# Kernel tuning notes

Hardware: AMD Instinct MI355X
Metric: run time of the kernel (lower is better)

The kernel has to match this reference:

```python
import jax, jax.numpy as jnp
import numpy as np

N_NODES = 50000
N_EDGES = 800000
F_IN = 32
HID = 64
K = 4  # Chebyshev order in GConvLSTM(node_features, hidden, 4)


def setup_inputs() -> dict:
    key = jax.random.key(0)
    ks = jax.random.split(key, 14)
    x = jax.random.normal(ks[0], (N_NODES, F_IN), dtype=jnp.float32)
    edge_index = jax.random.randint(ks[1], (2, N_EDGES), 0, N_NODES, dtype=jnp.int64)
    edge_weight = jax.random.uniform(ks[2], (N_EDGES,), dtype=jnp.float32)
    s = 0.05
    # gate order: i, f, c, o
    Wx = jax.random.normal(ks[3], (4, K, F_IN, HID), dtype=jnp.float32) * s  # ChebConv weights on x
    bx = jax.random.normal(ks[4], (4, HID), dtype=jnp.float32) * s          # ChebConv biases on x
    Wh = jax.random.normal(ks[5], (4, K, HID, HID), dtype=jnp.float32) * s  # ChebConv weights on h
    bh = jax.random.normal(ks[6], (4, HID), dtype=jnp.float32) * s          # ChebConv biases on h
    wc = jax.random.normal(ks[7], (3, HID), dtype=jnp.float32) * s          # peephole w_c_i, w_c_f, w_c_o
    bg = jax.random.normal(ks[8], (4, HID), dtype=jnp.float32) * s          # gate biases b_i, b_f, b_c, b_o
    lin_w = jax.random.normal(ks[9], (HID, 1), dtype=jnp.float32) * s
    lin_b = jax.random.normal(ks[10], (1,), dtype=jnp.float32) * s
    return {"x": x, "edge_index": edge_index, "edge_weight": edge_weight,
            "Wx": Wx, "bx": bx, "Wh": Wh, "bh": bh, "wc": wc, "bg": bg,
            "lin_w": lin_w, "lin_b": lin_b}


def _cheb_norm(edge_index, edge_weight, num_nodes):
    # ChebConv.__norm__, sym normalization, lambda_max=2.0:
    # L_hat off-diagonal = -D^{-1/2} A D^{-1/2}, diagonal = 0.
    src, dst = edge_index[0], edge_index[1]
    deg = jax.ops.segment_sum(edge_weight, src, num_segments=num_nodes)
    d_inv_sqrt = jnp.where(deg > 0, jax.lax.rsqrt(jnp.maximum(deg, 1e-30)), 0.0)
    norm = -d_inv_sqrt[src] * edge_weight * d_inv_sqrt[dst]
    return src, dst, norm


def _cheb_conv(v, src, dst, norm, W, b, num_nodes):
    # ChebConv forward: out = sum_k T_k(L_hat) v @ W[k] + b, with propagate
    # = segment_sum of norm * v[src] at dst.
    def prop(t):
        return jax.ops.segment_sum(norm[:, None] * t[src], dst, num_segments=num_nodes)
    Tx0 = v
    out = Tx0 @ W[0]
    Tx1 = prop(Tx0)
    out = out + Tx1 @ W[1]
    for k in range(2, W.shape[0]):
        Tx2 = 2.0 * prop(Tx1) - Tx0
        out = out + Tx2 @ W[k]
        Tx0, Tx1 = Tx1, Tx2
    return out + b


def reference(x, edge_index, edge_weight, Wx, bx, Wh, bh, wc, bg, lin_w, lin_b):
    N = x.shape[0]
    src, dst, norm = _cheb_norm(edge_index, edge_weight, N)
    H = jnp.zeros((N, Wh.shape[-1]), dtype=x.dtype)
    C = jnp.zeros((N, Wh.shape[-1]), dtype=x.dtype)

    def gate(g, v_state):
        return (_cheb_conv(x, src, dst, norm, Wx[g], bx[g], N)
                + _cheb_conv(v_state, src, dst, norm, Wh[g], bh[g], N))

    I = jax.nn.sigmoid(gate(0, H) + wc[0] * C + bg[0])
    F = jax.nn.sigmoid(gate(1, H) + wc[1] * C + bg[1])
    T = jnp.tanh(gate(2, H) + bg[2])
    C = F * C + I * T
    O = jax.nn.sigmoid(gate(3, H) + wc[2] * C + bg[3])
    H = O * jnp.tanh(C)
    # dropout(p=0.25) is identity at inference; linear head HID -> 1
    return H @ lin_w + lin_b
```

## Files before the change

### kernel.cpp

```cpp
#include <hip/hip_runtime.h>
#include <math.h>


#define NT 256
#define NCH 64
#define RSH 20480
#define RSF 20480

typedef __attribute__((ext_vector_type(8))) short short8v;
typedef __attribute__((ext_vector_type(8))) unsigned short ushort8v;
typedef __attribute__((ext_vector_type(4))) float f32x4;

__device__ __forceinline__ short f2bf(float f) {
    unsigned u = __float_as_uint(f);
    u += 0x7FFFu + ((u >> 16) & 1u);
    return (short)(u >> 16);
}
__device__ __forceinline__ float bf2f(unsigned short b) {
    return __uint_as_float((unsigned)b << 16);
}

__global__ __launch_bounds__(1024)
void k_front(const int* __restrict__ src, const int* __restrict__ dst,
             const float* __restrict__ w, float* __restrict__ degPart,
             unsigned short* __restrict__ cntPart,
             const float* __restrict__ Wx, short* __restrict__ P,
             const float* __restrict__ x, short* __restrict__ xb,
             int nE, int N, int histB, int n4) {
    __shared__ float    s_deg[RSH];
    __shared__ unsigned s_cnt2[RSH / 2];
    const int bid = blockIdx.x;
    if (bid >= histB) {
        int idx = (bid - histB) * 1024 + (int)threadIdx.x;
        if (idx < 12 * 4 * 64) {
            int lane = idx & 63;
            int kt = (idx >> 6) & 3;
            int nt = idx >> 8;
            int gate = (nt < 4) ? 0 : (nt < 8) ? 2 : 3;
            int h = (nt & 3) * 16 + (lane & 15);
            int fb = (lane >> 4) * 8;
            short8v v;
#pragma unroll
            for (int j = 0; j < 8; ++j)
                v[j] = f2bf(Wx[((size_t)(gate * 4 + kt) * 32 + fb + j) * 64 + h]);
            *(reinterpret_cast<short8v*>(P) + idx) = v;
            return;
        }
        int i = idx - 12 * 4 * 64;
        if (i >= n4) return;
        const float4 v = *reinterpret_cast<const float4*>(x + (size_t)i * 4);
        short4 rb;
        rb.x = f2bf(v.x); rb.y = f2bf(v.y); rb.z = f2bf(v.z); rb.w = f2bf(v.w);
        *reinterpret_cast<short4*>(xb + (size_t)i * 4) = rb;
        return;
    }
    const int r = bid / NCH, b = bid % NCH;
    const int base = r * RSH;
    for (int i = threadIdx.x; i < RSH; i += 1024) s_deg[i] = 0.f;
    for (int i = threadIdx.x; i < RSH / 2; i += 1024) s_cnt2[i] = 0u;
    __syncthreads();
    const int chunk = (nE + NCH - 1) / NCH;
    const int e0 = b * chunk, e1 = min(e0 + chunk, nE);
    for (int e = e0 + (int)threadIdx.x; e < e1; e += 1024) {
        int s = src[e], d = dst[e];
        unsigned so = (unsigned)(s - base), dof = (unsigned)(d - base);
        if (so < RSH) atomicAdd(&s_deg[so], w[e]);
        if (dof < RSH) atomicAdd(&s_cnt2[dof >> 1], 1u << ((dof & 1) * 16));
    }
    __syncthreads();
    const int lim = min(RSH, N - base);
    for (int i = threadIdx.x; i < lim; i += 1024)
        degPart[(size_t)b * N + base + i] = s_deg[i];
    unsigned* cp32 = reinterpret_cast<unsigned*>(cntPart + (size_t)b * N + base);
    const int pairs = lim >> 1;
    for (int i = threadIdx.x; i < pairs; i += 1024) cp32[i] = s_cnt2[i];
    if ((lim & 1) && threadIdx.x == 0)
        cntPart[(size_t)b * N + base + lim - 1] =
            (unsigned short)(s_cnt2[lim >> 1] & 0xFFFFu);
}

__global__ __launch_bounds__(NT)
void k_scan_merged(const float* __restrict__ degPart,
                   const unsigned short* __restrict__ cntPart,
                   float* __restrict__ dinv, int* __restrict__ cnt,
                   int* __restrict__ rowptr, int* __restrict__ partials,
                   int* __restrict__ flag, int* __restrict__ offs, int N) {
    __shared__ unsigned s_c[NCH * NT];
    __shared__ int sp[NT];
    const int t = threadIdx.x;
    const int n0 = blockIdx.x * (NT * 2) + t * 2;
    float d0 = 0.f, d1 = 0.f;
    int c0 = 0, c1 = 0;
    if (n0 < N) {
#pragma unroll 8
        for (int b = 0; b < NCH; ++b) {
            const float2 dv = *reinterpret_cast<const float2*>(degPart + (size_t)b * N + n0);
            d0 += dv.x; d1 += dv.y;
            unsigned cc = *reinterpret_cast<const unsigned*>(cntPart + (size_t)b * N + n0);
            s_c[b * NT + t] = cc;
            c0 += (int)(cc & 0xFFFFu); c1 += (int)(cc >> 16);
        }
        dinv[n0] = d0 > 0.f ? rsqrtf(d0) : 0.f;
        cnt[n0] = c0;
        if (n0 + 1 < N) {
            dinv[n0 + 1] = d1 > 0.f ? rsqrtf(d1) : 0.f;
            cnt[n0 + 1] = c1;
        } else c1 = 0;
    }
    int cs = c0 + c1;
    sp[t] = cs;
    __syncthreads();
    for (int off = 1; off < NT; off <<= 1) {
        int u = (t >= off) ? sp[t - off] : 0;
        __syncthreads();
        sp[t] += u;
        __syncthreads();
    }
    const int ex = sp[t] - cs;
    const int total = sp[NT - 1];
    __syncthreads();
    if (t == 0) {
        __hip_atomic_store(&partials[blockIdx.x], total, __ATOMIC_RELEASE,
                           __HIP_MEMORY_SCOPE_AGENT);
        atomicAdd(flag, 1);
        while (__hip_atomic_load(flag, __ATOMIC_ACQUIRE,
                                 __HIP_MEMORY_SCOPE_AGENT) < (int)gridDim.x)
            __builtin_amdgcn_s_sleep(1);
    }
    __syncthreads();
    int v = (t < (int)blockIdx.x)
                ? __hip_atomic_load(&partials[t], __ATOMIC_ACQUIRE,
                                    __HIP_MEMORY_SCOPE_AGENT)
                : 0;
    sp[t] = v;
    __syncthreads();
    for (int off = NT / 2; off > 0; off >>= 1) {
        if (t < off) sp[t] += sp[t + off];
        __syncthreads();
    }
    const int prefix = sp[0];
    if (n0 >= N) return;
    const bool has1 = (n0 + 1) < N;
    int s0 = ex + prefix;
    int s1 = has1 ? ex + c0 + prefix : 0;
    rowptr[n0] = s0;
    if (has1) rowptr[n0 + 1] = s1;
#pragma unroll 8
    for (int b = 0; b < NCH; ++b) {
        unsigned cc = s_c[b * NT + t];
        if (has1) {
            *reinterpret_cast<int2*>(offs + (size_t)b * N + n0) = make_int2(s0, s1);
        } else {
            offs[(size_t)b * N + n0] = s0;
        }
        s0 += (int)(cc & 0xFFFFu);
        s1 += (int)(cc >> 16);
    }
}

__global__ __launch_bounds__(1024)
void k_fill2(const int* __restrict__ src, const int* __restrict__ dst,
             const float* __restrict__ w, const float* __restrict__ dinv,
             const int* __restrict__ offs, int2* __restrict__ entries,
             int nE, int N) {
    __shared__ int s_cur[RSF];
    const int r = blockIdx.x / NCH, b = blockIdx.x % NCH;
    const int base = r * RSF;
    const int lim = min(RSF, N - base);
    for (int i = threadIdx.x; i < lim; i += 1024)
        s_cur[i] = offs[(size_t)b * N + base + i];
    __syncthreads();
    const int chunk = (nE + NCH - 1) / NCH;
    const int e0 = b * chunk, e1 = min(e0 + chunk, nE);
    for (int e = e0 + (int)threadIdx.x; e < e1; e += 1024) {
        int d = dst[e];
        unsigned dof = (unsigned)(d - base);
        if (dof < RSF) {
            int s = src[e];
            float nv = -dinv[s] * w[e] * dinv[d];
            int pos = atomicAdd(&s_cur[dof], 1);
            entries[pos] = make_int2(s, __float_as_int(nv));
        }
    }
}

__device__ __forceinline__ void bf8_fma(float* acc, ushort8v v, float s) {
#pragma unroll
    for (int j = 0; j < 8; ++j)
        acc[j] = fmaf(s, bf2f(v[j]), acc[j]);
}

__global__ __launch_bounds__(256)
void k_gather_bf(const unsigned short* __restrict__ tb,
                 const unsigned short* __restrict__ subb,
                 short* __restrict__ outb,
                 const int* __restrict__ rowptr, const int* __restrict__ cnt,
                 const int2* __restrict__ entries, float scale, int N) {
    int idx = blockIdx.x * blockDim.x + threadIdx.x;
    if (idx >= N * 16) return;
    int n = idx >> 4, tq = idx & 3, qr = (idx >> 2) & 3;
    int beg = rowptr[n], end = beg + cnt[n];
    float acc0[8] = {0, 0, 0, 0, 0, 0, 0, 0};
    float acc1[8] = {0, 0, 0, 0, 0, 0, 0, 0};
    int i = beg + qr;
    for (; i + 12 < end; i += 16) {
        int2 e0 = entries[i];
        int2 e1 = entries[i + 4];
        int2 e2 = entries[i + 8];
        int2 e3 = entries[i + 12];
        ushort8v v0 = *reinterpret_cast<const ushort8v*>(tb + (size_t)e0.x * 32 + tq * 8);
        ushort8v v1 = *reinterpret_cast<const ushort8v*>(tb + (size_t)e1.x * 32 + tq * 8);
        ushort8v v2 = *reinterpret_cast<const ushort8v*>(tb + (size_t)e2.x * 32 + tq * 8);
        ushort8v v3 = *reinterpret_cast<const ushort8v*>(tb + (size_t)e3.x * 32 + tq * 8);
        bf8_fma(acc0, v0, __int_as_float(e0.y));
        bf8_fma(acc1, v1, __int_as_float(e1.y));
        bf8_fma(acc0, v2, __int_as_float(e2.y));
        bf8_fma(acc1, v3, __int_as_float(e3.y));
    }
    for (; i < end; i += 4) {
        int2 e0 = entries[i];
        ushort8v v0 = *reinterpret_cast<const ushort8v*>(tb + (size_t)e0.x * 32 + tq * 8);
        bf8_fma(acc0, v0, __int_as_float(e0.y));
    }
    float r[8];
#pragma unroll
    for (int j = 0; j < 8; ++j) {
        r[j] = acc0[j] + acc1[j];
        r[j] += __shfl_xor(r[j], 4);
        r[j] += __shfl_xor(r[j], 8);
    }
    if (qr == 0) {
        if (subb) {
            ushort8v sv = *reinterpret_cast<const ushort8v*>(subb + (size_t)n * 32 + tq * 8);
#pragma unroll
            for (int j = 0; j < 8; ++j) r[j] = fmaf(scale, r[j], -bf2f(sv[j]));
        } else {
#pragma unroll
            for (int j = 0; j < 8; ++j) r[j] *= scale;
        }
        short8v rb;
#pragma unroll
        for (int j = 0; j < 8; ++j) rb[j] = f2bf(r[j]);
        *reinterpret_cast<short8v*>(outb + (size_t)n * 32 + tq * 8) = rb;
    }
}

__device__ __forceinline__ float sigf(float x) {
    return __builtin_amdgcn_rcpf(1.f + __builtin_amdgcn_exp2f(-1.4426950408889634f * x));
}
__device__ __forceinline__ float tanhf_fast(float x) {
    float e = __builtin_amdgcn_exp2f(2.8853900817779268f * x);
    return 1.f - 2.f * __builtin_amdgcn_rcpf(e + 1.f);
}

__global__ __launch_bounds__(256)
void k_final_g3(const short* __restrict__ xb, const short* __restrict__ t1b,
                const unsigned short* __restrict__ t2b,
                const short* __restrict__ P,
                const int* __restrict__ rowptr, const int* __restrict__ cnt,
                const int2* __restrict__ entries,
                const float* __restrict__ bx, const float* __restrict__ bh,
                const float* __restrict__ wc, const float* __restrict__ bg,
                const float* __restrict__ lin_w, const float* __restrict__ lin_b,
                float* __restrict__ out, int N) {
    const int wave = threadIdx.x >> 6, lane = threadIdx.x & 63;
    const int nb = blockIdx.x * 64 + wave * 16;
    const int rc = min(nb + (lane & 15), N - 1);
    const int ko = (lane >> 4) * 8;

    int beg = rowptr[rc], end = beg + cnt[rc];
    float acc0[8] = {0, 0, 0, 0, 0, 0, 0, 0};
    float acc1[8] = {0, 0, 0, 0, 0, 0, 0, 0};
    int i = beg;
    for (; i + 3 < end; i += 4) {
        int2 e0 = entries[i];
        int2 e1 = entries[i + 1];
        int2 e2 = entries[i + 2];
        int2 e3 = entries[i + 3];
        ushort8v v0 = *reinterpret_cast<const ushort8v*>(t2b + (size_t)e0.x * 32 + ko);
        ushort8v v1 = *reinterpret_cast<const ushort8v*>(t2b + (size_t)e1.x * 32 + ko);
        ushort8v v2 = *reinterpret_cast<const ushort8v*>(t2b + (size_t)e2.x * 32 + ko);
        ushort8v v3 = *reinterpret_cast<const ushort8v*>(t2b + (size_t)e3.x * 32 + ko);
        bf8_fma(acc0, v0, __int_as_float(e0.y));
        bf8_fma(acc1, v1, __int_as_float(e1.y));
        bf8_fma(acc0, v2, __int_as_float(e2.y));
        bf8_fma(acc1, v3, __int_as_float(e3.y));
    }
    for (; i < end; ++i) {
        int2 e0 = entries[i];
        ushort8v v0 = *reinterpret_cast<const ushort8v*>(t2b + (size_t)e0.x * 32 + ko);
        bf8_fma(acc0, v0, __int_as_float(e0.y));
    }

    short8v A0 = *reinterpret_cast<const short8v*>(xb  + (size_t)rc * 32 + ko);
    short8v A1 = *reinterpret_cast<const short8v*>(t1b + (size_t)rc * 32 + ko);
    short8v A2 = *reinterpret_cast<const short8v*>(
        reinterpret_cast<const short*>(t2b) + (size_t)rc * 32 + ko);
    short8v A3;
#pragma unroll
    for (int j = 0; j < 8; ++j)
        A3[j] = f2bf(2.f * (acc0[j] + acc1[j]) - bf2f((unsigned short)A1[j]));

    const short8v* Pv = reinterpret_cast<const short8v*>(P);
    f32x4 acc[12];
#pragma unroll
    for (int nt = 0; nt < 12; ++nt) {
        const short8v* Pb = Pv + (size_t)nt * 4 * 64 + lane;
        f32x4 a = {0.f, 0.f, 0.f, 0.f};
        a = __builtin_amdgcn_mfma_f32_16x16x32_bf16(A0, Pb[0],   a, 0, 0, 0);
        a = __builtin_amdgcn_mfma_f32_16x16x32_bf16(A1, Pb[64],  a, 0, 0, 0);
        a = __builtin_amdgcn_mfma_f32_16x16x32_bf16(A2, Pb[128], a, 0, 0, 0);
        a = __builtin_amdgcn_mfma_f32_16x16x32_bf16(A3, Pb[192], a, 0, 0, 0);
        acc[nt] = a;
    }

    const int hq = lane & 15;
    const int ng = lane >> 4;
    const float lb = lin_b[0];
    float p[4] = {0.f, 0.f, 0.f, 0.f};
#pragma unroll
    for (int ht = 0; ht < 4; ++ht) {
        int h = ht * 16 + hq;
        float bI = bx[h] + bh[h] + bg[h];
        float bC = bx[128 + h] + bh[128 + h] + bg[128 + h];
        float bO = bx[192 + h] + bh[192 + h] + bg[192 + h];
        float w2 = wc[128 + h];
        float lw = lin_w[h];
#pragma unroll
        for (int r = 0; r < 4; ++r) {
            float I = sigf(acc[ht][r] + bI);
            float T = tanhf_fast(acc[4 + ht][r] + bC);
            float C = I * T;
            float O = sigf(acc[8 + ht][r] + bO + w2 * C);
            float H = O * tanhf_fast(C);
            p[r] = fmaf(H, lw, p[r]);
        }
    }
#pragma unroll
    for (int r = 0; r < 4; ++r) {
        float v = p[r];
        v += __shfl_xor(v, 1);
        v += __shfl_xor(v, 2);
        v += __shfl_xor(v, 4);
        v += __shfl_xor(v, 8);
        if (hq == 0) {
            int n = nb + ng * 4 + r;
            if (n < N) out[n] = v + lb;
        }
    }
}

extern "C" void kernel_launch(void* const* d_in, const int* in_sizes, int n_in,
                              void* d_out, int out_size, void* d_ws, size_t ws_size,
                              hipStream_t stream) {
    const float* x   = (const float*)d_in[0];
    const int*   ei  = (const int*)d_in[1];
    const float* ew  = (const float*)d_in[2];
    const float* Wx  = (const float*)d_in[3];
    const float* bx  = (const float*)d_in[4];
    const float* bh  = (const float*)d_in[6];
    const float* wcp = (const float*)d_in[7];
    const float* bg  = (const float*)d_in[8];
    const float* lw  = (const float*)d_in[9];
    const float* lb  = (const float*)d_in[10];
    float* out = (float*)d_out;

    const int N  = in_sizes[0] / 32;
    const int nE = in_sizes[2];
    const int* src = ei;
    const int* dst = ei + nE;

    char* ws = (char*)d_ws;
    size_t off = 0;
    float* dinv    = (float*)(ws + off); off += (size_t)N * 4;
    int*   cnt     = (int*)(ws + off);   off += (size_t)N * 4;
    int*   rowptr  = (int*)(ws + off);   off += (size_t)N * 4;
    int*   partials= (int*)(ws + off);   off += 1024 * 4;
    int*   flag    = (int*)(ws + off);   off += 256;
    short* P       = (short*)(ws + off); off += 12 * 4 * 64 * 8 * 2;
    int2*  entries = (int2*)(ws + off);  off += (size_t)nE * 8;
    float* degPart = (float*)(ws + off); off += (size_t)NCH * N * 4;
    unsigned short* cntPart = (unsigned short*)(ws + off); off += (size_t)NCH * N * 2;
    short* xbuf    = (short*)(ws + off); off += (size_t)N * 32 * 2;
    short* Tx1b    = (short*)(ws + off); off += (size_t)N * 32 * 2;
    short* Tx2b    = (short*)(ws + off); off += (size_t)N * 32 * 2;

    int* offs = (int*)degPart;

    const int nRangeH = (N + RSH - 1) / RSH;
    const int nRangeF = (N + RSF - 1) / RSF;
    const int histB = nRangeH * NCH;
    const int n4 = N * 8;
    const int xbB = (12 * 4 * 64 + n4 + 1023) / 1024;
    const int nb2 = (N + NT * 2 - 1) / (NT * 2);

    hipMemsetAsync(flag, 0, 4, stream);
    k_front<<<histB + xbB, 1024, 0, stream>>>(src, dst, ew, degPart, cntPart,
                                              Wx, P, x, xbuf, nE, N, histB, n4);
    k_scan_merged<<<nb2, NT, 0, stream>>>(degPart, cntPart, dinv, cnt, rowptr,
                                          partials, flag, offs, N);
    k_fill2<<<nRangeF * NCH, 1024, 0, stream>>>(src, dst, ew, dinv, offs,
                                                entries, nE, N);

    const int gb = (N * 16 + NT - 1) / NT;
    k_gather_bf<<<gb, NT, 0, stream>>>((const unsigned short*)xbuf, nullptr,
                                       Tx1b, rowptr, cnt, entries, 1.f, N);
    k_gather_bf<<<gb, NT, 0, stream>>>((const unsigned short*)Tx1b,
                                       (const unsigned short*)xbuf,
                                       Tx2b, rowptr, cnt, entries, 2.f, N);

    const int fb = (N + 63) / 64;
    k_final_g3<<<fb, NT, 0, stream>>>(xbuf, Tx1b, (const unsigned short*)Tx2b, P,
                                      rowptr, cnt, entries, bx, bh, wcp, bg,
                                      lw, lb, out, N);
}
```

Before: 103.2 us.

## Split degree and count histograms; fill CSR with packed 16-bit rank counters

Separates the degree histogram (now 2 node ranges of 25600) from the in-degree count histogram, which now covers all nodes per block using packed 16-bit counters in one LDS array. The fill kernel likewise drops node-range partitioning: each of 64 blocks scans its edge chunk once, takes a per-destination rank from packed 16-bit LDS counters, and adds it to the precomputed offset. This removes the repeated edge scans that came from partitioning by node range. The cost is 100 KB of LDS per block, few blocks (64) doing the fill, and a scattered global read of offsets per edge.

```diff
diff --git a/kernel.cpp b/kernel.cpp
--- a/kernel.cpp
+++ b/kernel.cpp
@@ -4,8 +4,7 @@
 
 #define NT 256
 #define NCH 64
-#define RSH 20480
-#define RSF 20480
+#define RSD 25600
 
 typedef __attribute__((ext_vector_type(8))) short short8v;
 typedef __attribute__((ext_vector_type(8))) unsigned short ushort8v;
@@ -26,57 +25,65 @@
              unsigned short* __restrict__ cntPart,
              const float* __restrict__ Wx, short* __restrict__ P,
              const float* __restrict__ x, short* __restrict__ xb,
-             int nE, int N, int histB, int n4) {
-    __shared__ float    s_deg[RSH];
-    __shared__ unsigned s_cnt2[RSH / 2];
+             int nE, int N, int degB, int n4) {
+    __shared__ unsigned smem[RSD];
     const int bid = blockIdx.x;
-    if (bid >= histB) {
-        int idx = (bid - histB) * 1024 + (int)threadIdx.x;
-        if (idx < 12 * 4 * 64) {
-            int lane = idx & 63;
-            int kt = (idx >> 6) & 3;
-            int nt = idx >> 8;
-            int gate = (nt < 4) ? 0 : (nt < 8) ? 2 : 3;
-            int h = (nt & 3) * 16 + (lane & 15);
-            int fb = (lane >> 4) * 8;
-            short8v v;
-#pragma unroll
-            for (int j = 0; j < 8; ++j)
-                v[j] = f2bf(Wx[((size_t)(gate * 4 + kt) * 32 + fb + j) * 64 + h]);
-            *(reinterpret_cast<short8v*>(P) + idx) = v;
-            return;
-        }
-        int i = idx - 12 * 4 * 64;
-        if (i >= n4) return;
-        const float4 v = *reinterpret_cast<const float4*>(x + (size_t)i * 4);
-        short4 rb;
-        rb.x = f2bf(v.x); rb.y = f2bf(v.y); rb.z = f2bf(v.z); rb.w = f2bf(v.w);
-        *reinterpret_cast<short4*>(xb + (size_t)i * 4) = rb;
+    const int chunk = (nE + NCH - 1) / NCH;
+
+    if (bid < degB) {
+        float* s_deg = reinterpret_cast<float*>(smem);
+        const int r = bid / NCH, b = bid % NCH;
+        const int base = r * RSD;
+        for (int i = threadIdx.x; i < RSD; i += 1024) s_deg[i] = 0.f;
+        __syncthreads();
+        const int e0 = b * chunk, e1 = min(e0 + chunk, nE);
+        for (int e = e0 + (int)threadIdx.x; e < e1; e += 1024) {
+            unsigned so = (unsigned)(src[e] - base);
+            if (so < RSD) atomicAdd(&s_deg[so], w[e]);
+        }
+        __syncthreads();
+        const int lim = min(RSD, N - base);
+        for (int i = threadIdx.x; i < lim; i += 1024)
+            degPart[(size_t)b * N + base + i] = s_deg[i];
         return;
     }
-    const int r = bid / NCH, b = bid % NCH;
-    const int base = r * RSH;
-    for (int i = threadIdx.x; i < RSH; i += 1024) s_deg[i] = 0.f;
-    for (int i = threadIdx.x; i < RSH / 2; i += 1024) s_cnt2[i] = 0u;
-    __syncthreads();
-    const int chunk = (nE + NCH - 1) / NCH;
-    const int e0 = b * chunk, e1 = min(e0 + chunk, nE);
-    for (int e = e0 + (int)threadIdx.x; e < e1; e += 1024) {
-        int s = src[e], d = dst[e];
-        unsigned so = (unsigned)(s - base), dof = (unsigned)(d - base);
-        if (so < RSH) atomicAdd(&s_deg[so], w[e]);
-        if (dof < RSH) atomicAdd(&s_cnt2[dof >> 1], 1u << ((dof & 1) * 16));
-    }
-    __syncthreads();
-    const int lim = min(RSH, N - base);
-    for (int i = threadIdx.x; i < lim; i += 1024)
-        degPart[(size_t)b * N + base + i] = s_deg[i];
-    unsigned* cp32 = reinterpret_cast<unsigned*>(cntPart + (size_t)b * N + base);
-    const int pairs = lim >> 1;
-    for (int i = threadIdx.x; i < pairs; i += 1024) cp32[i] = s_cnt2[i];
-    if ((lim & 1) && threadIdx.x == 0)
-        cntPart[(size_t)b * N + base + lim - 1] =
-            (unsigned short)(s_cnt2[lim >> 1] & 0xFFFFu);
+    if (bid < degB + NCH) {
+        unsigned* s_cnt2 = smem;
+        const int b = bid - degB;
+        const int pairsN = (N + 1) >> 1;
+        for (int i = threadIdx.x; i < pairsN; i += 1024) s_cnt2[i] = 0u;
+        __syncthreads();
+        const int e0 = b * chunk, e1 = min(e0 + chunk, nE);
+        for (int e = e0 + (int)threadIdx.x; e < e1; e += 1024) {
+            unsigned d = (unsigned)dst[e];
+            atomicAdd(&s_cnt2[d >> 1], 1u << ((d & 1) * 16));
+        }
+        __syncthreads();
+        unsigned* cp32 = reinterpret_cast<unsigned*>(cntPart + (size_t)b * N);
+        for (int i = threadIdx.x; i < pairsN; i += 1024) cp32[i] = s_cnt2[i];
+        return;
+    }
+    int idx = (bid - degB - NCH) * 1024 + (int)threadIdx.x;
+    if (idx < 12 * 4 * 64) {
+        int lane = idx & 63;
+        int kt = (idx >> 6) & 3;
+        int nt = idx >> 8;
+        int gate = (nt < 4) ? 0 : (nt < 8) ? 2 : 3;
+        int h = (nt & 3) * 16 + (lane & 15);
+        int fb = (lane >> 4) * 8;
+        short8v v;
+#pragma unroll
+        for (int j = 0; j < 8; ++j)
+            v[j] = f2bf(Wx[((size_t)(gate * 4 + kt) * 32 + fb + j) * 64 + h]);
+        *(reinterpret_cast<short8v*>(P) + idx) = v;
+        return;
+    }
+    int i = idx - 12 * 4 * 64;
+    if (i >= n4) return;
+    const float4 v = *reinterpret_cast<const float4*>(x + (size_t)i * 4);
+    short4 rb;
+    rb.x = f2bf(v.x); rb.y = f2bf(v.y); rb.z = f2bf(v.z); rb.w = f2bf(v.w);
+    *reinterpret_cast<short4*>(xb + (size_t)i * 4) = rb;
 }
 
 __global__ __launch_bounds__(NT)
@@ -159,28 +166,26 @@
 }
 
 __global__ __launch_bounds__(1024)
-void k_fill2(const int* __restrict__ src, const int* __restrict__ dst,
-             const float* __restrict__ w, const float* __restrict__ dinv,
-             const int* __restrict__ offs, int2* __restrict__ entries,
-             int nE, int N) {
-    __shared__ int s_cur[RSF];
-    const int r = blockIdx.x / NCH, b = blockIdx.x % NCH;
-    const int base = r * RSF;
-    const int lim = min(RSF, N - base);
-    for (int i = threadIdx.x; i < lim; i += 1024)
-        s_cur[i] = offs[(size_t)b * N + base + i];
+void k_fill(const int* __restrict__ src, const int* __restrict__ dst,
+            const float* __restrict__ w, const float* __restrict__ dinv,
+            const int* __restrict__ offs, int2* __restrict__ entries,
+            int nE, int N) {
+    __shared__ unsigned s_rank[RSD];
+    const int b = blockIdx.x;
+    const int pairsN = (N + 1) >> 1;
+    for (int i = threadIdx.x; i < pairsN; i += 1024) s_rank[i] = 0u;
     __syncthreads();
     const int chunk = (nE + NCH - 1) / NCH;
     const int e0 = b * chunk, e1 = min(e0 + chunk, nE);
+    const int* offb = offs + (size_t)b * N;
     for (int e = e0 + (int)threadIdx.x; e < e1; e += 1024) {
-        int d = dst[e];
-        unsigned dof = (unsigned)(d - base);
-        if (dof < RSF) {
-            int s = src[e];
-            float nv = -dinv[s] * w[e] * dinv[d];
-            int pos = atomicAdd(&s_cur[dof], 1);
-            entries[pos] = make_int2(s, __float_as_int(nv));
-        }
+        int s = src[e];
+        unsigned d = (unsigned)dst[e];
+        float nv = -dinv[s] * w[e] * dinv[d];
+        unsigned sh = (d & 1) * 16;
+        unsigned old = atomicAdd(&s_rank[d >> 1], 1u << sh);
+        int rank = (int)((old >> sh) & 0xFFFFu);
+        entries[offb[d] + rank] = make_int2(s, __float_as_int(nv));
     }
 }
 
@@ -387,20 +392,18 @@
 
     int* offs = (int*)degPart;
 
-    const int nRangeH = (N + RSH - 1) / RSH;
-    const int nRangeF = (N + RSF - 1) / RSF;
-    const int histB = nRangeH * NCH;
+    const int nRangeD = (N + RSD - 1) / RSD;
+    const int degB = nRangeD * NCH;
     const int n4 = N * 8;
     const int xbB = (12 * 4 * 64 + n4 + 1023) / 1024;
     const int nb2 = (N + NT * 2 - 1) / (NT * 2);
 
     hipMemsetAsync(flag, 0, 4, stream);
-    k_front<<<histB + xbB, 1024, 0, stream>>>(src, dst, ew, degPart, cntPart,
-                                              Wx, P, x, xbuf, nE, N, histB, n4);
+    k_front<<<degB + NCH + xbB, 1024, 0, stream>>>(src, dst, ew, degPart, cntPart,
+                                                   Wx, P, x, xbuf, nE, N, degB, n4);
     k_scan_merged<<<nb2, NT, 0, stream>>>(degPart, cntPart, dinv, cnt, rowptr,
                                           partials, flag, offs, N);
-    k_fill2<<<nRangeF * NCH, 1024, 0, stream>>>(src, dst, ew, dinv, offs,
-                                                entries, nE, N);
+    k_fill<<<NCH, 1024, 0, stream>>>(src, dst, ew, dinv, offs, entries, nE, N);
 
     const int gb = (N * 16 + NT - 1) / NT;
     k_gather_bf<<<gb, NT, 0, stream>>>((const unsigned short*)xbuf, nullptr,
```

Measured after the change: 141.4 us. +37.1%, slower.
